# Kernel optimization log

Hardware: AMD Instinct MI355X
Metric: run time of the kernel (lower is better)

## Reference

```python
import jax, jax.numpy as jnp
import numpy as np

CH = 512
COND = 1280
HEADS = 8
GROUPS = CH // 8
EPS = 1e-5


def conv2d(x, w, b, pad):
    y = jax.lax.conv_general_dilated(
        x, w, window_strides=(1, 1), padding=[(pad, pad), (pad, pad)],
        dimension_numbers=('NCHW', 'OIHW', 'NCHW'))
    return y + b[None, :, None, None]


def group_norm(x, gamma, beta, groups, eps=EPS):
    b, c, h, w = x.shape
    xg = x.reshape(b, groups, c // groups, h, w)
    mu = xg.mean(axis=(2, 3, 4), keepdims=True)
    var = xg.var(axis=(2, 3, 4), keepdims=True)
    xn = ((xg - mu) * jax.lax.rsqrt(var + eps)).reshape(b, c, h, w)
    return xn * gamma[None, :, None, None] + beta[None, :, None, None]


def setup_inputs() -> dict:
    key = jax.random.key(0)
    ks = jax.random.split(key, 20)
    s = 0.05
    inp = {
        'x': jax.random.normal(ks[0], (8, CH, 32, 32), jnp.float32),
        'conditioning': jax.random.normal(ks[1], (8, COND), jnp.float32),
        # ResBlock params
        'c1w': jax.random.normal(ks[2], (CH, CH, 3, 3), jnp.float32) * s,
        'c1b': jnp.zeros((CH,), jnp.float32),
        'g1w': jnp.ones((CH,), jnp.float32),
        'g1b': jnp.zeros((CH,), jnp.float32),
        'c2w': jax.random.normal(ks[3], (CH, CH, 3, 3), jnp.float32) * s,
        'c2b': jnp.zeros((CH,), jnp.float32),
        'g2w': jnp.ones((CH,), jnp.float32),
        'g2b': jnp.zeros((CH,), jnp.float32),
        'cpw': jax.random.normal(ks[4], (CH, COND), jnp.float32) * s,
        'cpb': jnp.zeros((CH,), jnp.float32),
        'rpw': jax.random.normal(ks[5], (CH, CH, 1, 1), jnp.float32) * s,
        'rpb': jnp.zeros((CH,), jnp.float32),
        # Attention params (1x1 convs)
        'qw': jax.random.normal(ks[6], (CH, CH, 1, 1), jnp.float32) * s,
        'qb': jnp.zeros((CH,), jnp.float32),
        'kw': jax.random.normal(ks[7], (CH, CH, 1, 1), jnp.float32) * s,
        'kb': jnp.zeros((CH,), jnp.float32),
        'vw': jax.random.normal(ks[8], (CH, CH, 1, 1), jnp.float32) * s,
        'vb': jnp.zeros((CH,), jnp.float32),
        'ow': jax.random.normal(ks[9], (CH, CH, 1, 1), jnp.float32) * s,
        'ob': jnp.zeros((CH,), jnp.float32),
    }
    return inp


def reference(x, conditioning, c1w, c1b, g1w, g1b, c2w, c2b, g2w, g2b,
              cpw, cpb, rpw, rpb, qw, qb, kw, kb, vw, vb, ow, ob):
    # --- ResBlock ---
    residual = conv2d(x, rpw, rpb, 0)
    h = conv2d(x, c1w, c1b, 1)
    h = group_norm(h, g1w, g1b, GROUPS)
    h = jax.nn.silu(h)
    h = conv2d(h, c2w, c2b, 1)
    h = group_norm(h, g2w, g2b, GROUPS)
    cond = conditioning @ cpw.T + cpb  # [B, C]
    h = h * (1.0 + cond[:, :, None, None]) + residual

    # --- SpatialSelfAttention ---
    b, c, hh, ww = h.shape
    d = c // HEADS
    scale = d ** (-0.5)
    q = conv2d(h, qw, qb, 0).reshape(b, HEADS, d, hh * ww)
    k = conv2d(h, kw, kb, 0).reshape(b, HEADS, d, hh * ww)
    v = conv2d(h, vw, vb, 0).reshape(b, HEADS, d, hh * ww)
    attn = jnp.einsum('bhdn,bhdm->bhnm', q, k) * scale  # [B,H,N,N]
    attn = jax.nn.softmax(attn, axis=-1)
    out = jnp.einsum('bhnm,bhdm->bhdn', attn, v).reshape(b, c, hh, ww)
    return conv2d(out, ow, ob, 0) + h
```

## Files before the change

### kernel.cpp

```cpp
#include <hip/hip_runtime.h>
#include <hip/hip_bf16.h>

typedef unsigned short u16;
typedef unsigned long long u64;
typedef __attribute__((ext_vector_type(8))) short bf8;
typedef __attribute__((ext_vector_type(4))) short bf4;
typedef __attribute__((ext_vector_type(4))) float f32x4;

#define CH_ 512
#define NSP 1024
#define NB 8
#define CONDDIM 1280
#define NGROUP 64
#define HEADS_ 8
#define HD 64
#define PR 34
#define PPB (PR*PR)
#define QSCALE 0.18033688011112042f

#define VWAIT(N) asm volatile("s_waitcnt vmcnt(" #N ")" ::: "memory")
#define SCHEDB __builtin_amdgcn_sched_barrier(0)
#define BARRIER do { SCHEDB; __builtin_amdgcn_s_barrier(); SCHEDB; } while (0)

__device__ __forceinline__ u16 f2bf(float f) {
  union { float f; unsigned u; } v; v.f = f;
  unsigned u = v.u;
  return (u16)((u + 0x7fffu + ((u >> 16) & 1u)) >> 16);
}

__device__ __forceinline__ unsigned cvt_pk_bf16(float lo, float hi) {
  unsigned r;
  asm volatile("v_cvt_pk_bf16_f32 %0, %1, %2" : "=v"(r) : "v"(lo), "v"(hi));
  return r;
}

__device__ __forceinline__ f32x4 mfma_bf16(bf8 a, bf8 b, f32x4 c) {
  return __builtin_amdgcn_mfma_f32_16x16x32_bf16(a, b, c, 0, 0, 0);
}

__device__ __forceinline__ void gload16(const void* g, void* l) {
  __builtin_amdgcn_global_load_lds((const __attribute__((address_space(1))) void*)g,
                                   (__attribute__((address_space(3))) void*)l, 16, 0, 0);
}


__global__ __launch_bounds__(1024) void pack_x_kernel(const float* __restrict__ x, u16* __restrict__ xp) {
  __shared__ float t[32][33];
  int b = blockIdx.z;
  int c0 = blockIdx.y * 32, p0 = blockIdx.x * 32;
  int tx = threadIdx.x & 31, ty = threadIdx.x >> 5;
  t[ty][tx] = x[((size_t)b * CH_ + c0 + ty) * NSP + p0 + tx];
  __syncthreads();
  int p = p0 + ty;
  int y = p >> 5, xc = p & 31;
  xp[((size_t)b * PPB + (size_t)(y + 1) * PR + xc + 1) * CH_ + c0 + tx] = f2bf(t[tx][ty]);
}

__global__ __launch_bounds__(256) void border_zero_kernel(u16* __restrict__ a, u16* __restrict__ b) {
  int id = blockIdx.x * 256 + threadIdx.x;
  if (id >= NB * 132 * 64) return;
  int ch8 = id & 63;
  int rest = id >> 6;
  int bidx = rest % 132;
  int bb = rest / 132;
  int r, c;
  if (bidx < 34)       { r = 0;          c = bidx; }
  else if (bidx < 68)  { r = 33;         c = bidx - 34; }
  else if (bidx < 100) { r = bidx - 67;  c = 0; }
  else                 { r = bidx - 99;  c = 33; }
  size_t off = ((size_t)bb * PPB + (size_t)r * PR + c) * CH_ + ch8 * 8;
  const bf8 z = {0, 0, 0, 0, 0, 0, 0, 0};
  *(bf8*)(a + off) = z;
  *(bf8*)(b + off) = z;
}

__global__ __launch_bounds__(256) void pack_w3_kernel(const float* __restrict__ wA, const float* __restrict__ wB,
                                                      u16* __restrict__ dA, u16* __restrict__ dB) {
  int id = blockIdx.x * 256 + threadIdx.x;
  if (id >= 9 * 64 * CH_) return;
  const float* w = blockIdx.y ? wB : wA;
  u16* wp = blockIdx.y ? dB : dA;
  int co = id & (CH_ - 1);
  int cib = (id >> 9) & 63;
  int t = id >> 15;
  int dy = t / 3, dx = t % 3;
  bf8 v;
#pragma unroll
  for (int j = 0; j < 8; j++) {
    int ci = cib * 8 + j;
    v[j] = (short)f2bf(w[(((size_t)co * CH_ + ci) * 3 + dy) * 3 + dx]);
  }
  *(bf8*)(wp + ((size_t)(t * 64 + cib) * CH_ + co) * 8) = v;
}

__global__ __launch_bounds__(256) void pack_w1_kernel(
    const float* __restrict__ s0, const float* __restrict__ s1, const float* __restrict__ s2,
    const float* __restrict__ s3, const float* __restrict__ s4,
    u16* __restrict__ d0, u16* __restrict__ d1, u16* __restrict__ d2,
    u16* __restrict__ d3, u16* __restrict__ d4) {
  int id = blockIdx.x * 256 + threadIdx.x;
  if (id >= 64 * CH_) return;
  const float* w; u16* wp;
  switch (blockIdx.y) {
    case 0: w = s0; wp = d0; break;
    case 1: w = s1; wp = d1; break;
    case 2: w = s2; wp = d2; break;
    case 3: w = s3; wp = d3; break;
    default: w = s4; wp = d4; break;
  }
  int co = id & (CH_ - 1);
  int cib = id >> 9;
  bf8 v;
#pragma unroll
  for (int j = 0; j < 8; j++) v[j] = (short)f2bf(w[(size_t)co * CH_ + cib * 8 + j]);
  *(bf8*)(wp + ((size_t)cib * CH_ + co) * 8) = v;
}

__global__ __launch_bounds__(256) void cond_kernel(const float* __restrict__ cd, const float* __restrict__ cpw,
                                                   const float* __restrict__ cpb, float* __restrict__ cond) {
  int b = blockIdx.y;
  int c = blockIdx.x * 4 + (threadIdx.x >> 6);
  int lane = threadIdx.x & 63;
  const float* wrow = cpw + (size_t)c * CONDDIM;
  const float* crow = cd + (size_t)b * CONDDIM;
  float s = 0.f;
  for (int i = lane; i < CONDDIM; i += 64) s += crow[i] * wrow[i];
#pragma unroll
  for (int m = 32; m > 0; m >>= 1) s += __shfl_xor(s, m, 64);
  if (lane == 0) cond[b * CH_ + c] = s + cpb[c];
}

template <int TAPS, int PIN, int EPI>
__global__ __launch_bounds__(256, 3) void conv_kernel(
    const u16* __restrict__ in, const u16* __restrict__ wp, const float* __restrict__ bias,
    float* __restrict__ outf, const float* __restrict__ addf,
    u16* __restrict__ o0, u16* __restrict__ o1, u16* __restrict__ o2,
    const float* __restrict__ b0, const float* __restrict__ b1, const float* __restrict__ b2,
    const u16* __restrict__ wp2, float* __restrict__ outf2, const float* __restrict__ bias2) {
  constexpr int LDSZ = (TAPS == 9) ? (2 * 14336 + 3 * 12288 + (EPI == 6 ? 2 * 4096 : 0))
                                   : (4 * 8192 + 4 * 4096);
  __shared__ char lds[LDSZ];
  char* ldsA = lds;
  char* ldsB = lds + ((TAPS == 9) ? 2 * 14336 : 4 * 8192);
  char* ldsR = lds + 2 * 14336 + 3 * 12288;

  const int b = blockIdx.z;
  int seg = 0, coy = blockIdx.y;
  if constexpr (EPI == 5) { seg = coy >> 3; coy &= 7; }
  const int co0 = coy * 64;
  const int p0 = blockIdx.x * 128;
  const int tid = threadIdx.x;
  const int lane = tid & 63, wid = tid >> 6;
  const int wv = wid >> 1, wc = wid & 1;
  const int l15 = lane & 15, lhi = lane >> 4;

  const char* aSrc;
  if constexpr (TAPS == 9) {
    aSrc = (const char*)in + ((size_t)b * PPB + (size_t)blockIdx.x * 4 * PR) * 1024;
  } else if constexpr (PIN) {
    aSrc = (const char*)in + (size_t)b * PPB * 1024;
  } else {
    aSrc = (const char*)in + ((size_t)b * NSP + p0) * 1024;
  }
  const char* bSrc = (const char*)wp + (size_t)((EPI == 5) ? seg * 524288 : 0) + co0 * 16;
  const char* rSrc = (const char*)wp2 + co0 * 16;

  const int pB = ((tid >> 6) * 512 + (tid & 63)) * 16;
  int pA0, pA1, pA3 = 0;
  if constexpr (TAPS == 9) {
    int r0 = tid >> 2;
    int c0s = (tid & 3) ^ ((r0 >> 1) & 3);
    pA0 = (r0 << 10) + (c0s << 4);
    int r3 = 192 + ((tid & 127) >> 2);
    int c3s = (tid & 3) ^ ((r3 >> 1) & 3);
    pA3 = (r3 << 10) + (c3s << 4);
    pA1 = 0;
  } else {
    int a0 = (tid >> 2), a1 = 64 + (tid >> 2);
    int cs = (tid & 3) ^ (((tid >> 2) >> 1) & 3);
    if constexpr (PIN) {
      int pp0 = p0 + a0, pp1 = p0 + a1;
      int g0 = ((pp0 >> 5) + 1) * PR + (pp0 & 31) + 1;
      int g1 = ((pp1 >> 5) + 1) * PR + (pp1 & 31) + 1;
      pA0 = (g0 << 10) + (cs << 4);
      pA1 = (g1 << 10) + (cs << 4);
    } else {
      pA0 = (a0 << 10) + (cs << 4);
      pA1 = (a1 << 10) + (cs << 4);
    }
  }

  const int rowbA = (TAPS == 9) ? (wv * 68 + l15) : (wv * 64 + l15);
  const int aAddr = rowbA * 64 + ((lhi ^ ((l15 >> 1) & 3)) << 4);
  const int bAddr = (lhi * 64 + wc * 32 + l15) * 16;

  f32x4 acc[4][2], accR[4][2];
#pragma unroll
  for (int m = 0; m < 4; m++)
#pragma unroll
    for (int n = 0; n < 2; n++) { acc[m][n] = {0.f, 0.f, 0.f, 0.f}; accR[m][n] = {0.f, 0.f, 0.f, 0.f}; }

  if constexpr (TAPS == 9) {
    gload16(aSrc + pA0,          ldsA + (wid << 10));
    gload16(aSrc + pA0 + 65536,  ldsA + 4096 + (wid << 10));
    gload16(aSrc + pA0 + 131072, ldsA + 8192 + (wid << 10));
    gload16(aSrc + pA3,          ldsA + 12288 + ((wid & 1) << 10));
    gload16(bSrc + (size_t)(0 * 64) * 8192 + pB, ldsB + (wid << 10));
    gload16(bSrc + (size_t)(1 * 64) * 8192 + pB, ldsB + 4096 + (wid << 10));
    gload16(bSrc + (size_t)(2 * 64) * 8192 + pB, ldsB + 8192 + (wid << 10));
    gload16(bSrc + (size_t)(3 * 64) * 8192 + pB, ldsB + 12288 + (wid << 10));
    gload16(bSrc + (size_t)(4 * 64) * 8192 + pB, ldsB + 12288 + 4096 + (wid << 10));
    gload16(bSrc + (size_t)(5 * 64) * 8192 + pB, ldsB + 12288 + 8192 + (wid << 10));
    if constexpr (EPI == 6) {
      gload16(rSrc + pB, ldsR + (wid << 10));
      VWAIT(4);
    } else {
      VWAIT(3);
    }
    BARRIER;

#define AREAD(Ab_, K) (*(const bf8*)((Ab_) + (rowbA + (K)) * 64 + ((lhi ^ (((rowbA + (K)) >> 1) & 3)) << 4)))

#define PH3(KC, T, AS) do {                                                             \
    const int kcn_ = ((KC) < 15) ? (KC) + 1 : 15;                                       \
    if constexpr ((T) == 0) {                                                           \
      gload16(bSrc + (size_t)(6 * 64 + (KC) * 4) * 8192 + pB, ldsB + 24576 + (wid << 10)); \
      gload16(bSrc + (size_t)(7 * 64 + (KC) * 4) * 8192 + pB, ldsB + 24576 + 4096 + (wid << 10)); \
      gload16(bSrc + (size_t)(8 * 64 + (KC) * 4) * 8192 + pB, ldsB + 24576 + 8192 + (wid << 10)); \
      gload16(aSrc + kcn_ * 64 + pA0,         ldsA + (1 - (AS)) * 14336 + (wid << 10)); \
      gload16(aSrc + kcn_ * 64 + pA0 + 65536, ldsA + (1 - (AS)) * 14336 + 4096 + (wid << 10)); \
    } else if constexpr ((T) == 1) {                                                    \
      gload16(bSrc + (size_t)(0 * 64 + kcn_ * 4) * 8192 + pB, ldsB + (wid << 10));      \
      gload16(bSrc + (size_t)(1 * 64 + kcn_ * 4) * 8192 + pB, ldsB + 4096 + (wid << 10)); \
      gload16(bSrc + (size_t)(2 * 64 + kcn_ * 4) * 8192 + pB, ldsB + 8192 + (wid << 10)); \
      gload16(aSrc + kcn_ * 64 + pA0 + 131072, ldsA + (1 - (AS)) * 14336 + 8192 + (wid << 10)); \
      if constexpr (EPI == 6)                                                           \
        if ((KC) < 15)                                                                  \
          gload16(rSrc + (size_t)kcn_ * 32768 + pB, ldsR + (kcn_ & 1) * 4096 + (wid << 10)); \
    } else {                                                                            \
      gload16(bSrc + (size_t)(3 * 64 + kcn_ * 4) * 8192 + pB, ldsB + 12288 + (wid << 10)); \
      gload16(bSrc + (size_t)(4 * 64 + kcn_ * 4) * 8192 + pB, ldsB + 12288 + 4096 + (wid << 10)); \
      gload16(bSrc + (size_t)(5 * 64 + kcn_ * 4) * 8192 + pB, ldsB + 12288 + 8192 + (wid << 10)); \
      gload16(aSrc + kcn_ * 64 + pA3, ldsA + (1 - (AS)) * 14336 + 12288 + ((wid & 1) << 10)); \
    }                                                                                   \
    SCHEDB;                                                                             \
    {                                                                                   \
      const char* Ab_ = ldsA + (AS) * 14336;                                            \
      const char* Bb_ = ldsB + (T) * 12288;                                             \
      bf8 af_[3][4], bq_[3][2];                                                         \
      _Pragma("unroll")                                                                 \
      for (int tt = 0; tt < 3; tt++) {                                                  \
        const int DT_ = (T) * 34 + tt;                                                  \
        af_[tt][0] = AREAD(Ab_, DT_ + 0);                                               \
        af_[tt][1] = AREAD(Ab_, DT_ + 16);                                              \
        af_[tt][2] = AREAD(Ab_, DT_ + 34);                                              \
        af_[tt][3] = AREAD(Ab_, DT_ + 50);                                              \
        bq_[tt][0] = *(const bf8*)(Bb_ + tt * 4096 + 0   + bAddr);                      \
        bq_[tt][1] = *(const bf8*)(Bb_ + tt * 4096 + 256 + bAddr);                      \
      }                                                                                 \
      __builtin_amdgcn_s_setprio(1);                                                    \
      _Pragma("unroll")                                                                 \
      for (int tt = 0; tt < 3; tt++)                                                    \
        _Pragma("unroll")                                                               \
        for (int m = 0; m < 4; m++) {                                                   \
          acc[m][0] = mfma_bf16(af_[tt][m], bq_[tt][0], acc[m][0]);                     \
          acc[m][1] = mfma_bf16(af_[tt][m], bq_[tt][1], acc[m][1]);                     \
        }                                                                               \
      if constexpr (EPI == 6 && (T) == 1) {                                             \
        bf8 rq0 = *(const bf8*)(ldsR + ((KC) & 1) * 4096 + 0   + bAddr);                \
        bf8 rq1 = *(const bf8*)(ldsR + ((KC) & 1) * 4096 + 256 + bAddr);                \
        _Pragma("unroll")                                                               \
        for (int m = 0; m < 4; m++) {                                                   \
          accR[m][0] = mfma_bf16(af_[1][m], rq0, accR[m][0]);                           \
          accR[m][1] = mfma_bf16(af_[1][m], rq1, accR[m][1]);                           \
        }                                                                               \
      }                                                                                 \
      __builtin_amdgcn_s_setprio(0);                                                    \
    }                                                                                   \
    if constexpr ((T) == 0) { VWAIT(5); }                                               \
    else if constexpr ((T) == 1) {                                                      \
      if constexpr (EPI == 6) { VWAIT(5); } else { VWAIT(4); }                          \
    } else { VWAIT(4); }                                                                \
    BARRIER;                                                                            \
  } while (0)

    for (int kc2 = 0; kc2 < 8; kc2++) {
      PH3(kc2 * 2,     0, 0); PH3(kc2 * 2,     1, 0); PH3(kc2 * 2,     2, 0);
      PH3(kc2 * 2 + 1, 0, 1); PH3(kc2 * 2 + 1, 1, 1); PH3(kc2 * 2 + 1, 2, 1);
    }
#undef PH3
#undef AREAD
  } else {
    gload16(aSrc + pA0,         ldsA + (wid << 10));
    gload16(aSrc + pA1,         ldsA + 4096 + (wid << 10));
    gload16(bSrc + pB,          ldsB + (wid << 10));
    gload16(aSrc + 64 + pA0,    ldsA + 8192 + (wid << 10));
    gload16(aSrc + 64 + pA1,    ldsA + 8192 + 4096 + (wid << 10));
    gload16(bSrc + 32768 + pB,  ldsB + 4096 + (wid << 10));
    VWAIT(3);
    BARRIER;

#define PH1(KC, S) do {                                                                 \
    constexpr int S2 = ((S) + 2) & 3;                                                   \
    const int kcn_ = ((KC) + 2 < 16) ? (KC) + 2 : 15;                                   \
    gload16(bSrc + (size_t)kcn_ * 32768 + pB, ldsB + S2 * 4096 + (wid << 10));          \
    gload16(aSrc + kcn_ * 64 + pA0, ldsA + S2 * 8192 + (wid << 10));                    \
    gload16(aSrc + kcn_ * 64 + pA1, ldsA + S2 * 8192 + 4096 + (wid << 10));             \
    SCHEDB;                                                                             \
    bf8 af0 = *(const bf8*)(ldsA + (S) * 8192 + 0    + aAddr);                          \
    bf8 af1 = *(const bf8*)(ldsA + (S) * 8192 + 1024 + aAddr);                          \
    bf8 af2 = *(const bf8*)(ldsA + (S) * 8192 + 2048 + aAddr);                          \
    bf8 af3 = *(const bf8*)(ldsA + (S) * 8192 + 3072 + aAddr);                          \
    bf8 bq0 = *(const bf8*)(ldsB + (S) * 4096 + 0   + bAddr);                           \
    bf8 bq1 = *(const bf8*)(ldsB + (S) * 4096 + 256 + bAddr);                           \
    __builtin_amdgcn_s_setprio(1);                                                      \
    acc[0][0] = mfma_bf16(af0, bq0, acc[0][0]);                                         \
    acc[0][1] = mfma_bf16(af0, bq1, acc[0][1]);                                         \
    acc[1][0] = mfma_bf16(af1, bq0, acc[1][0]);                                         \
    acc[1][1] = mfma_bf16(af1, bq1, acc[1][1]);                                         \
    acc[2][0] = mfma_bf16(af2, bq0, acc[2][0]);                                         \
    acc[2][1] = mfma_bf16(af2, bq1, acc[2][1]);                                         \
    acc[3][0] = mfma_bf16(af3, bq0, acc[3][0]);                                         \
    acc[3][1] = mfma_bf16(af3, bq1, acc[3][1]);                                         \
    __builtin_amdgcn_s_setprio(0);                                                      \
    VWAIT(3);                                                                           \
    BARRIER;                                                                            \
  } while (0)

    for (int kc4 = 0; kc4 < 4; kc4++) {
      PH1(kc4 * 4 + 0, 0); PH1(kc4 * 4 + 1, 1); PH1(kc4 * 4 + 2, 2); PH1(kc4 * 4 + 3, 3);
    }
#undef PH1
  }

  VWAIT(0);

#pragma unroll
  for (int m = 0; m < 4; m++) {
    int pbase = p0 + wv * 64 + m * 16 + lhi * 4;
#pragma unroll
    for (int n = 0; n < 2; n++) {
      int co = co0 + wc * 32 + n * 16 + l15;
      if constexpr (EPI == 0) {
        float bv = bias[co];
#pragma unroll
        for (int r = 0; r < 4; r++)
          outf[((size_t)b * NSP + pbase + r) * CH_ + co] = acc[m][n][r] + bv;
      } else if constexpr (EPI == 6) {
        float bv = bias[co];
        float rv = bias2[co];
#pragma unroll
        for (int r = 0; r < 4; r++) {
          size_t idx = ((size_t)b * NSP + pbase + r) * CH_ + co;
          outf[idx]  = acc[m][n][r] + bv;
          outf2[idx] = accR[m][n][r] + rv;
        }
      } else if constexpr (EPI == 2) {
        float bv = bias[co];
        f32x4 v;
#pragma unroll
        for (int r = 0; r < 4; r++)
          v[r] = acc[m][n][r] + bv + addf[((size_t)b * NSP + pbase + r) * CH_ + co];
        *(f32x4*)(outf + ((size_t)b * CH_ + co) * NSP + pbase) = v;
      } else {
        if (seg == 0) {
          float bv = b0[co];
#pragma unroll
          for (int r = 0; r < 4; r++)
            o0[((size_t)b * NSP + pbase + r) * CH_ + co] = f2bf((acc[m][n][r] + bv) * QSCALE);
        } else if (seg == 1) {
          float bv = b1[co];
#pragma unroll
          for (int r = 0; r < 4; r++)
            o1[((size_t)b * NSP + pbase + r) * CH_ + co] = f2bf(acc[m][n][r] + bv);
        } else {
          float bv = b2[co];
          union { bf4 v; u64 u; } pk4;
#pragma unroll
          for (int r = 0; r < 4; r++) pk4.v[r] = (short)f2bf(acc[m][n][r] + bv);
          int np = (pbase & ~31) | ((pbase & 12) << 1) | ((pbase & 16) >> 2);
          *(u64*)(o2 + ((size_t)b * CH_ + co) * NSP + np) = pk4.u;
        }
      }
    }
  }
}

template <int MODE>
__global__ __launch_bounds__(256) void gn_kernel(
    const float* __restrict__ in, const float* __restrict__ gw, const float* __restrict__ gb,
    const float* __restrict__ cond, const float* __restrict__ resid,
    float* __restrict__ outf, u16* __restrict__ outb) {
  int b = blockIdx.y, g = blockIdx.x;
  int tid = threadIdx.x;
  int c = g * 8 + (tid & 7);
  int prow = tid >> 3;
  const float* base = in + (size_t)b * NSP * CH_ + c;
  float v[32];
  float s = 0.f, ss = 0.f;
#pragma unroll
  for (int i = 0; i < 32; i++) {
    v[i] = base[(size_t)(prow + i * 32) * CH_];
    s += v[i]; ss += v[i] * v[i];
  }
  __shared__ float rs[256], rss[256];
  rs[tid] = s; rss[tid] = ss;
  __syncthreads();
  for (int off = 128; off > 0; off >>= 1) {
    if (tid < off) { rs[tid] += rs[tid + off]; rss[tid] += rss[tid + off]; }
    __syncthreads();
  }
  float mean = rs[0] * (1.f / 8192.f);
  float var = rss[0] * (1.f / 8192.f) - mean * mean;
  float inv = rsqrtf(var + 1e-5f);
  float gamma = gw[c], beta = gb[c];
  float cm = 0.f;
  if (MODE == 1) cm = 1.f + cond[b * CH_ + c];
#pragma unroll
  for (int i = 0; i < 32; i++) {
    int p = prow + i * 32;
    float y = (v[i] - mean) * inv * gamma + beta;
    if (MODE == 0) {
      float sg = 1.f / (1.f + __expf(-y));
      int yy = p >> 5, xc = p & 31;
      outb[((size_t)b * PPB + (size_t)(yy + 1) * PR + xc + 1) * CH_ + c] = f2bf(y * sg);
    } else {
      size_t idx = ((size_t)b * NSP + p) * CH_ + c;
      float z = y * cm + resid[idx];
      outf[idx] = z;
      outb[idx] = f2bf(z);
    }
  }
}

__global__ __launch_bounds__(256, 2) void attn_kernel(const u16* __restrict__ q, const u16* __restrict__ k,
                                                      const u16* __restrict__ vT, u16* __restrict__ ao) {
  int bid = blockIdx.x;
  int swz = (bid & 7) * 64 + (bid >> 3);
  int b = swz >> 6;
  int head = (swz >> 3) & 7;
  int qt = swz & 7;
  int tid = threadIdx.x, lane = tid & 63, wid = tid >> 6;
  int l15 = lane & 15, lhi = lane >> 4;
  int cb = head * HD;
  int q0 = qt * 128 + wid * 32;

  const char* qp = (const char*)(q + (size_t)b * NSP * CH_ + cb);
  const char* kp = (const char*)(k + (size_t)b * NSP * CH_ + cb);
  const char* vp = (const char*)(vT + ((size_t)b * CH_ + cb) * NSP);

  __shared__ u16 Ksh[3][64 * 64];
  __shared__ u16 Vsh[3][64 * 64];

  bf8 aq[2][2];
#pragma unroll
  for (int qh = 0; qh < 2; qh++)
#pragma unroll
    for (int ks = 0; ks < 2; ks++)
      aq[qh][ks] = *(const bf8*)(qp + ((size_t)(q0 + qh * 16 + l15) * CH_ + ks * 32 + lhi * 8) * 2);

  const bf8 ones8 = {16256, 16256, 16256, 16256, 16256, 16256, 16256, 16256};

  f32x4 o[2][4], osum[2];
#pragma unroll
  for (int qh = 0; qh < 2; qh++) {
    osum[qh] = {0.f, 0.f, 0.f, 0.f};
#pragma unroll
    for (int n = 0; n < 4; n++) o[qh][n] = {0.f, 0.f, 0.f, 0.f};
  }

  auto stage = [&](int kt, int buf) {
#pragma unroll
    for (int t = 0; t < 2; t++) {
      int i = wid * 2 + t;
      int chunk = i * 64 + lane;
      int r = chunk >> 3, c = chunk & 7;
      gload16(kp + (size_t)(kt * 64 + r) * 1024 + (size_t)((c ^ (r & 7)) * 16),
              (char*)Ksh[buf] + i * 1024);
    }
#pragma unroll
    for (int t = 0; t < 2; t++) {
      int i = wid * 2 + t;
      int chunk = i * 64 + lane;
      int r = chunk >> 3, c = chunk & 7;
      gload16(vp + (size_t)r * 2048 + (size_t)(kt * 128) + (size_t)((c ^ (r & 7)) * 16),
              (char*)Vsh[buf] + i * 1024);
    }
  };

  auto qk = [&](int buf, f32x4 (&sacc)[2][4]) {
    const char* Kb = (const char*)Ksh[0] + buf * 8192;
#pragma unroll
    for (int qh = 0; qh < 2; qh++)
#pragma unroll
      for (int kf = 0; kf < 4; kf++) sacc[qh][kf] = {0.f, 0.f, 0.f, 0.f};
#pragma unroll
    for (int kf = 0; kf < 4; kf++) {
      bf8 ak[2];
#pragma unroll
      for (int ks = 0; ks < 2; ks++)
        ak[ks] = *(const bf8*)(Kb + (size_t)(kf * 16 + l15) * 128 + (((ks * 4 + lhi) ^ (l15 & 7)) * 16));
#pragma unroll
      for (int qh = 0; qh < 2; qh++)
#pragma unroll
        for (int ks = 0; ks < 2; ks++)
          sacc[qh][kf] = mfma_bf16(ak[ks], aq[qh][ks], sacc[qh][kf]);
    }
  };

  auto smpv = [&](int buf, f32x4 (&sacc)[2][4]) {
    const char* Vb = (const char*)Vsh[0] + buf * 8192;
    unsigned pk[2][4][2];
#pragma unroll
    for (int qh = 0; qh < 2; qh++)
#pragma unroll
      for (int kf = 0; kf < 4; kf++) {
        f32x4 pv;
#pragma unroll
        for (int r = 0; r < 4; r++) pv[r] = exp2f(sacc[qh][kf][r]);
        pk[qh][kf][0] = cvt_pk_bf16(pv[0], pv[1]);
        pk[qh][kf][1] = cvt_pk_bf16(pv[2], pv[3]);
      }
#pragma unroll
    for (int g = 0; g < 2; g++) {
      union { bf8 v8; unsigned u[4]; } ap[2];
#pragma unroll
      for (int qh = 0; qh < 2; qh++) {
        ap[qh].u[0] = pk[qh][2 * g][0];
        ap[qh].u[1] = pk[qh][2 * g][1];
        ap[qh].u[2] = pk[qh][2 * g + 1][0];
        ap[qh].u[3] = pk[qh][2 * g + 1][1];
      }
#pragma unroll
      for (int nf2 = 0; nf2 < 4; nf2++) {
        int row = nf2 * 16 + l15;
        bf8 bv8 = *(const bf8*)(Vb + (size_t)row * 128 + (((4 * g + lhi) ^ (l15 & 7)) * 16));
#pragma unroll
        for (int qh = 0; qh < 2; qh++)
          o[qh][nf2] = mfma_bf16(ap[qh].v8, bv8, o[qh][nf2]);
      }
#pragma unroll
      for (int qh = 0; qh < 2; qh++)
        osum[qh] = mfma_bf16(ap[qh].v8, ones8, osum[qh]);
    }
  };

  stage(0, 0);
  stage(1, 1);
  VWAIT(4);
  BARRIER;

  f32x4 saccA[2][4], saccB[2][4];
  qk(0, saccA);

  int bc = 0;
  for (int kt2 = 0; kt2 < 8; kt2++) {
    {
      int kt = 2 * kt2;
      int bn = (bc == 2) ? 0 : bc + 1;
      int bs = (bn == 2) ? 0 : bn + 1;
      VWAIT(0);
      BARRIER;
      qk(bn, saccB);
      if (kt < 14) stage(kt + 2, bs);
      smpv(bc, saccA);
      bc = bn;
    }
    {
      int kt = 2 * kt2 + 1;
      if (kt < 15) {
        int bn = (bc == 2) ? 0 : bc + 1;
        int bs = (bn == 2) ? 0 : bn + 1;
        VWAIT(0);
        BARRIER;
        qk(bn, saccA);
        if (kt < 14) stage(kt + 2, bs);
        smpv(bc, saccB);
        bc = bn;
      } else {
        smpv(bc, saccB);
      }
    }
  }

#pragma unroll
  for (int qh = 0; qh < 2; qh++) {
    float linv[4];
#pragma unroll
    for (int r = 0; r < 4; r++) linv[r] = 1.f / osum[qh][r];
#pragma unroll
    for (int nf2 = 0; nf2 < 4; nf2++)
#pragma unroll
      for (int r = 0; r < 4; r++) {
        float val = o[qh][nf2][r] * linv[r];
        ao[((size_t)b * NSP + q0 + qh * 16 + lhi * 4 + r) * CH_ + cb + nf2 * 16 + l15] = f2bf(val);
      }
  }
}


extern "C" void kernel_launch(void* const* d_in, const int* in_sizes, int n_in,
                              void* d_out, int out_size, void* d_ws, size_t ws_size,
                              hipStream_t stream) {
  const float* x    = (const float*)d_in[0];
  const float* cnd  = (const float*)d_in[1];
  const float* c1w  = (const float*)d_in[2];
  const float* c1b  = (const float*)d_in[3];
  const float* g1w  = (const float*)d_in[4];
  const float* g1b  = (const float*)d_in[5];
  const float* c2w  = (const float*)d_in[6];
  const float* c2b  = (const float*)d_in[7];
  const float* g2w  = (const float*)d_in[8];
  const float* g2b  = (const float*)d_in[9];
  const float* cpw  = (const float*)d_in[10];
  const float* cpb  = (const float*)d_in[11];
  const float* rpw  = (const float*)d_in[12];
  const float* rpb  = (const float*)d_in[13];
  const float* qw   = (const float*)d_in[14];
  const float* qb   = (const float*)d_in[15];
  const float* kw   = (const float*)d_in[16];
  const float* kb   = (const float*)d_in[17];
  const float* vw   = (const float*)d_in[18];
  const float* vb   = (const float*)d_in[19];
  const float* ow   = (const float*)d_in[20];
  const float* ob   = (const float*)d_in[21];
  float* out = (float*)d_out;

  char* ws = (char*)d_ws;
  size_t off = 0;
  auto alloc = [&](size_t bytes) -> char* {
    char* p = ws + off;
    off = (off + bytes + 255) & ~(size_t)255;
    return p;
  };
  const size_t ACT_F = (size_t)NB * NSP * CH_ * 4;
  const size_t ACT_B = (size_t)NB * NSP * CH_ * 2;
  const size_t PAD_B = (size_t)NB * PPB * CH_ * 2;

  u16* xp    = (u16*)alloc(PAD_B);
  u16* h1p   = (u16*)alloc(PAD_B);
  u16* w1p   = (u16*)alloc((size_t)9 * CH_ * CH_ * 2);
  u16* w2p   = (u16*)alloc((size_t)9 * CH_ * CH_ * 2);
  u16* wrp   = (u16*)alloc((size_t)CH_ * CH_ * 2);
  u16* wqkv  = (u16*)alloc((size_t)3 * CH_ * CH_ * 2);
  u16* wop   = (u16*)alloc((size_t)CH_ * CH_ * 2);
  float* cndv = (float*)alloc((size_t)NB * CH_ * 4);
  float* resid = (float*)alloc(ACT_F);
  float* h12  = (float*)alloc(ACT_F);
  u16* hb    = (u16*)alloc(ACT_B);
  u16* qbuf  = (u16*)alloc(ACT_B);
  u16* kbuf  = (u16*)alloc(ACT_B);
  u16* vTb   = (u16*)alloc(ACT_B);
  u16* aob   = (u16*)alloc(ACT_B);
  if (off > ws_size) return;

  dim3 tgrid(NSP / 32, CH_ / 32, NB);
  border_zero_kernel<<<(NB * 132 * 64 + 255) / 256, 256, 0, stream>>>(xp, h1p);
  pack_x_kernel<<<tgrid, 1024, 0, stream>>>(x, xp);
  pack_w3_kernel<<<dim3((9 * 64 * CH_ + 255) / 256, 2), 256, 0, stream>>>(c1w, c2w, w1p, w2p);
  pack_w1_kernel<<<dim3((64 * CH_) / 256, 5), 256, 0, stream>>>(
      rpw, qw, kw, vw, ow,
      wrp, wqkv, wqkv + (size_t)CH_ * CH_, wqkv + (size_t)2 * CH_ * CH_, wop);
  cond_kernel<<<dim3(CH_ / 4, NB), 256, 0, stream>>>(cnd, cpw, cpb, cndv);

  dim3 ggrid(NSP / 128, CH_ / 64, NB);
  dim3 qgrid(NSP / 128, 3 * CH_ / 64, NB);
  conv_kernel<9, 1, 6><<<ggrid, 256, 0, stream>>>(xp, w1p, c1b, h12, nullptr,
                                                  nullptr, nullptr, nullptr, nullptr, nullptr, nullptr,
                                                  wrp, resid, rpb);
  gn_kernel<0><<<dim3(NGROUP, NB), 256, 0, stream>>>(h12, g1w, g1b, nullptr, nullptr, nullptr, h1p);
  conv_kernel<9, 1, 0><<<ggrid, 256, 0, stream>>>(h1p, w2p, c2b, h12, nullptr,
                                                  nullptr, nullptr, nullptr, nullptr, nullptr, nullptr,
                                                  nullptr, nullptr, nullptr);
  gn_kernel<1><<<dim3(NGROUP, NB), 256, 0, stream>>>(h12, g2w, g2b, cndv, resid, h12, hb);
  conv_kernel<1, 0, 5><<<qgrid, 256, 0, stream>>>(hb, wqkv, nullptr, nullptr, nullptr,
                                                  qbuf, kbuf, vTb, qb, kb, vb,
                                                  nullptr, nullptr, nullptr);
  attn_kernel<<<512, 256, 0, stream>>>(qbuf, kbuf, vTb, aob);
  conv_kernel<1, 0, 2><<<ggrid, 256, 0, stream>>>(aob, wop, ob, out, h12,
                                                  nullptr, nullptr, nullptr, nullptr, nullptr, nullptr,
                                                  nullptr, nullptr, nullptr);
}
```

Baseline: 239.1 us.

## Merge prep kernels into one launch and store conv outputs as bf16 for groupnorm

Five setup kernels (border zeroing, input packing, weight packing and the conditioning projection) become a single prep_kernel launch that dispatches on block index. The two 3x3 convs now write bf16 pre-norm activations instead of fp32, which halves the traffic into the groupnorm kernels. The groupnorm kernels are rewritten to load 8 channels per thread as 16-byte vectors and store vectorized outputs. The cost is bf16 rounding before the groupnorm statistics, which may reduce accuracy.

Result: faster. 221.3 us (-7.4%).

```diff
diff --git a/kernel.cpp b/kernel.cpp
--- a/kernel.cpp
+++ b/kernel.cpp
@@ -28,6 +28,10 @@
   return (u16)((u + 0x7fffu + ((u >> 16) & 1u)) >> 16);
 }
 
+__device__ __forceinline__ float b2f(u16 x) {
+  union { unsigned u; float f; } v; v.u = ((unsigned)x) << 16; return v.f;
+}
+
 __device__ __forceinline__ unsigned cvt_pk_bf16(float lo, float hi) {
   unsigned r;
   asm volatile("v_cvt_pk_bf16_f32 %0, %1, %2" : "=v"(r) : "v"(lo), "v"(hi));
@@ -43,91 +47,99 @@
                                    (__attribute__((address_space(3))) void*)l, 16, 0, 0);
 }
 
-
-__global__ __launch_bounds__(1024) void pack_x_kernel(const float* __restrict__ x, u16* __restrict__ xp) {
+__global__ __launch_bounds__(256) void prep_kernel(
+    const float* __restrict__ x, u16* __restrict__ xp, u16* __restrict__ h1p,
+    const float* __restrict__ c1w, const float* __restrict__ c2w,
+    u16* __restrict__ w1p, u16* __restrict__ w2p,
+    const float* __restrict__ rpw, const float* __restrict__ qw, const float* __restrict__ kw,
+    const float* __restrict__ vw, const float* __restrict__ ow,
+    u16* __restrict__ wrp, u16* __restrict__ wq, u16* __restrict__ wk,
+    u16* __restrict__ wv, u16* __restrict__ wo,
+    const float* __restrict__ cd, const float* __restrict__ cpw,
+    const float* __restrict__ cpb, float* __restrict__ cond) {
   __shared__ float t[32][33];
-  int b = blockIdx.z;
-  int c0 = blockIdx.y * 32, p0 = blockIdx.x * 32;
-  int tx = threadIdx.x & 31, ty = threadIdx.x >> 5;
-  t[ty][tx] = x[((size_t)b * CH_ + c0 + ty) * NSP + p0 + tx];
-  __syncthreads();
-  int p = p0 + ty;
-  int y = p >> 5, xc = p & 31;
-  xp[((size_t)b * PPB + (size_t)(y + 1) * PR + xc + 1) * CH_ + c0 + tx] = f2bf(t[tx][ty]);
-}
-
-__global__ __launch_bounds__(256) void border_zero_kernel(u16* __restrict__ a, u16* __restrict__ b) {
-  int id = blockIdx.x * 256 + threadIdx.x;
-  if (id >= NB * 132 * 64) return;
-  int ch8 = id & 63;
-  int rest = id >> 6;
-  int bidx = rest % 132;
-  int bb = rest / 132;
-  int r, c;
-  if (bidx < 34)       { r = 0;          c = bidx; }
-  else if (bidx < 68)  { r = 33;         c = bidx - 34; }
-  else if (bidx < 100) { r = bidx - 67;  c = 0; }
-  else                 { r = bidx - 99;  c = 33; }
-  size_t off = ((size_t)bb * PPB + (size_t)r * PR + c) * CH_ + ch8 * 8;
-  const bf8 z = {0, 0, 0, 0, 0, 0, 0, 0};
-  *(bf8*)(a + off) = z;
-  *(bf8*)(b + off) = z;
-}
-
-__global__ __launch_bounds__(256) void pack_w3_kernel(const float* __restrict__ wA, const float* __restrict__ wB,
-                                                      u16* __restrict__ dA, u16* __restrict__ dB) {
-  int id = blockIdx.x * 256 + threadIdx.x;
-  if (id >= 9 * 64 * CH_) return;
-  const float* w = blockIdx.y ? wB : wA;
-  u16* wp = blockIdx.y ? dB : dA;
-  int co = id & (CH_ - 1);
-  int cib = (id >> 9) & 63;
-  int t = id >> 15;
-  int dy = t / 3, dx = t % 3;
-  bf8 v;
-#pragma unroll
-  for (int j = 0; j < 8; j++) {
-    int ci = cib * 8 + j;
-    v[j] = (short)f2bf(w[(((size_t)co * CH_ + ci) * 3 + dy) * 3 + dx]);
-  }
-  *(bf8*)(wp + ((size_t)(t * 64 + cib) * CH_ + co) * 8) = v;
-}
-
-__global__ __launch_bounds__(256) void pack_w1_kernel(
-    const float* __restrict__ s0, const float* __restrict__ s1, const float* __restrict__ s2,
-    const float* __restrict__ s3, const float* __restrict__ s4,
-    u16* __restrict__ d0, u16* __restrict__ d1, u16* __restrict__ d2,
-    u16* __restrict__ d3, u16* __restrict__ d4) {
-  int id = blockIdx.x * 256 + threadIdx.x;
-  if (id >= 64 * CH_) return;
-  const float* w; u16* wp;
-  switch (blockIdx.y) {
-    case 0: w = s0; wp = d0; break;
-    case 1: w = s1; wp = d1; break;
-    case 2: w = s2; wp = d2; break;
-    case 3: w = s3; wp = d3; break;
-    default: w = s4; wp = d4; break;
-  }
-  int co = id & (CH_ - 1);
-  int cib = id >> 9;
-  bf8 v;
-#pragma unroll
-  for (int j = 0; j < 8; j++) v[j] = (short)f2bf(w[(size_t)co * CH_ + cib * 8 + j]);
-  *(bf8*)(wp + ((size_t)cib * CH_ + co) * 8) = v;
-}
-
-__global__ __launch_bounds__(256) void cond_kernel(const float* __restrict__ cd, const float* __restrict__ cpw,
-                                                   const float* __restrict__ cpb, float* __restrict__ cond) {
-  int b = blockIdx.y;
-  int c = blockIdx.x * 4 + (threadIdx.x >> 6);
-  int lane = threadIdx.x & 63;
-  const float* wrow = cpw + (size_t)c * CONDDIM;
-  const float* crow = cd + (size_t)b * CONDDIM;
-  float s = 0.f;
-  for (int i = lane; i < CONDDIM; i += 64) s += crow[i] * wrow[i];
-#pragma unroll
-  for (int m = 32; m > 0; m >>= 1) s += __shfl_xor(s, m, 64);
-  if (lane == 0) cond[b * CH_ + c] = s + cpb[c];
+  int bid = blockIdx.x;
+  int tid = threadIdx.x;
+  if (bid < 4096) {
+    int px = bid & 31, py = (bid >> 5) & 15, b = bid >> 9;
+    int c0 = py * 32, p0 = px * 32;
+    int tx = tid & 31, ty = tid >> 5;
+#pragma unroll
+    for (int i = 0; i < 4; i++) {
+      int row = ty + i * 8;
+      t[row][tx] = x[((size_t)b * CH_ + c0 + row) * NSP + p0 + tx];
+    }
+    __syncthreads();
+#pragma unroll
+    for (int i = 0; i < 4; i++) {
+      int pr = ty + i * 8;
+      int p = p0 + pr;
+      int y = p >> 5, xc = p & 31;
+      xp[((size_t)b * PPB + (size_t)(y + 1) * PR + xc + 1) * CH_ + c0 + tx] = f2bf(t[tx][pr]);
+    }
+  } else if (bid < 4360) {
+    int id = (bid - 4096) * 256 + tid;
+    int ch8 = id & 63;
+    int rest = id >> 6;
+    int bidx = rest % 132;
+    int bb = rest / 132;
+    int r, c;
+    if (bidx < 34)       { r = 0;          c = bidx; }
+    else if (bidx < 68)  { r = 33;         c = bidx - 34; }
+    else if (bidx < 100) { r = bidx - 67;  c = 0; }
+    else                 { r = bidx - 99;  c = 33; }
+    size_t off = ((size_t)bb * PPB + (size_t)r * PR + c) * CH_ + ch8 * 8;
+    const bf8 z = {0, 0, 0, 0, 0, 0, 0, 0};
+    *(bf8*)(xp + off) = z;
+    *(bf8*)(h1p + off) = z;
+  } else if (bid < 6664) {
+    int id2 = bid - 4360;
+    int which = (id2 >= 1152) ? 1 : 0;
+    int id = (id2 - which * 1152) * 256 + tid;
+    const float* w = which ? c2w : c1w;
+    u16* wp = which ? w2p : w1p;
+    int co = id & (CH_ - 1);
+    int cib = (id >> 9) & 63;
+    int tt = id >> 15;
+    int dy = tt / 3, dx = tt % 3;
+    bf8 v;
+#pragma unroll
+    for (int j = 0; j < 8; j++) {
+      int ci = cib * 8 + j;
+      v[j] = (short)f2bf(w[(((size_t)co * CH_ + ci) * 3 + dy) * 3 + dx]);
+    }
+    *(bf8*)(wp + ((size_t)(tt * 64 + cib) * CH_ + co) * 8) = v;
+  } else if (bid < 7304) {
+    int id3 = bid - 6664;
+    int which = id3 >> 7;
+    int id = (id3 & 127) * 256 + tid;
+    const float* w; u16* wp;
+    switch (which) {
+      case 0: w = rpw; wp = wrp; break;
+      case 1: w = qw;  wp = wq;  break;
+      case 2: w = kw;  wp = wk;  break;
+      case 3: w = vw;  wp = wv;  break;
+      default: w = ow; wp = wo;  break;
+    }
+    int co = id & (CH_ - 1);
+    int cib = id >> 9;
+    bf8 v;
+#pragma unroll
+    for (int j = 0; j < 8; j++) v[j] = (short)f2bf(w[(size_t)co * CH_ + cib * 8 + j]);
+    *(bf8*)(wp + ((size_t)cib * CH_ + co) * 8) = v;
+  } else {
+    int id4 = bid - 7304;
+    int b = id4 >> 7;
+    int c = (id4 & 127) * 4 + (tid >> 6);
+    int lane = tid & 63;
+    const float* wrow = cpw + (size_t)c * CONDDIM;
+    const float* crow = cd + (size_t)b * CONDDIM;
+    float s = 0.f;
+    for (int i = lane; i < CONDDIM; i += 64) s += crow[i] * wrow[i];
+#pragma unroll
+    for (int m = 32; m > 0; m >>= 1) s += __shfl_xor(s, m, 64);
+    if (lane == 0) cond[b * CH_ + c] = s + cpb[c];
+  }
 }
 
 template <int TAPS, int PIN, int EPI>
@@ -137,7 +149,7 @@
     u16* __restrict__ o0, u16* __restrict__ o1, u16* __restrict__ o2,
     const float* __restrict__ b0, const float* __restrict__ b1, const float* __restrict__ b2,
     const u16* __restrict__ wp2, float* __restrict__ outf2, const float* __restrict__ bias2) {
-  constexpr int LDSZ = (TAPS == 9) ? (2 * 14336 + 3 * 12288 + (EPI == 6 ? 2 * 4096 : 0))
+  constexpr int LDSZ = (TAPS == 9) ? (2 * 14336 + 3 * 12288 + (EPI == 8 ? 2 * 4096 : 0))
                                    : (4 * 8192 + 4 * 4096);
   __shared__ char lds[LDSZ];
   char* ldsA = lds;
@@ -211,7 +223,7 @@
     gload16(bSrc + (size_t)(3 * 64) * 8192 + pB, ldsB + 12288 + (wid << 10));
     gload16(bSrc + (size_t)(4 * 64) * 8192 + pB, ldsB + 12288 + 4096 + (wid << 10));
     gload16(bSrc + (size_t)(5 * 64) * 8192 + pB, ldsB + 12288 + 8192 + (wid << 10));
-    if constexpr (EPI == 6) {
+    if constexpr (EPI == 8) {
       gload16(rSrc + pB, ldsR + (wid << 10));
       VWAIT(4);
     } else {
@@ -234,7 +246,7 @@
       gload16(bSrc + (size_t)(1 * 64 + kcn_ * 4) * 8192 + pB, ldsB + 4096 + (wid << 10)); \
       gload16(bSrc + (size_t)(2 * 64 + kcn_ * 4) * 8192 + pB, ldsB + 8192 + (wid << 10)); \
       gload16(aSrc + kcn_ * 64 + pA0 + 131072, ldsA + (1 - (AS)) * 14336 + 8192 + (wid << 10)); \
-      if constexpr (EPI == 6)                                                           \
+      if constexpr (EPI == 8)                                                           \
         if ((KC) < 15)                                                                  \
           gload16(rSrc + (size_t)kcn_ * 32768 + pB, ldsR + (kcn_ & 1) * 4096 + (wid << 10)); \
     } else {                                                                            \
@@ -266,7 +278,7 @@
           acc[m][0] = mfma_bf16(af_[tt][m], bq_[tt][0], acc[m][0]);                     \
           acc[m][1] = mfma_bf16(af_[tt][m], bq_[tt][1], acc[m][1]);                     \
         }                                                                               \
-      if constexpr (EPI == 6 && (T) == 1) {                                             \
+      if constexpr (EPI == 8 && (T) == 1) {                                             \
         bf8 rq0 = *(const bf8*)(ldsR + ((KC) & 1) * 4096 + 0   + bAddr);                \
         bf8 rq1 = *(const bf8*)(ldsR + ((KC) & 1) * 4096 + 256 + bAddr);                \
         _Pragma("unroll")                                                               \
@@ -279,7 +291,7 @@
     }                                                                                   \
     if constexpr ((T) == 0) { VWAIT(5); }                                               \
     else if constexpr ((T) == 1) {                                                      \
-      if constexpr (EPI == 6) { VWAIT(5); } else { VWAIT(4); }                          \
+      if constexpr (EPI == 8) { VWAIT(5); } else { VWAIT(4); }                          \
     } else { VWAIT(4); }                                                                \
     BARRIER;                                                                            \
   } while (0)
@@ -341,18 +353,18 @@
 #pragma unroll
     for (int n = 0; n < 2; n++) {
       int co = co0 + wc * 32 + n * 16 + l15;
-      if constexpr (EPI == 0) {
+      if constexpr (EPI == 7) {
         float bv = bias[co];
 #pragma unroll
         for (int r = 0; r < 4; r++)
-          outf[((size_t)b * NSP + pbase + r) * CH_ + co] = acc[m][n][r] + bv;
-      } else if constexpr (EPI == 6) {
+          o0[((size_t)b * NSP + pbase + r) * CH_ + co] = f2bf(acc[m][n][r] + bv);
+      } else if constexpr (EPI == 8) {
         float bv = bias[co];
         float rv = bias2[co];
 #pragma unroll
         for (int r = 0; r < 4; r++) {
           size_t idx = ((size_t)b * NSP + pbase + r) * CH_ + co;
-          outf[idx]  = acc[m][n][r] + bv;
+          o0[idx]    = f2bf(acc[m][n][r] + bv);
           outf2[idx] = accR[m][n][r] + rv;
         }
       } else if constexpr (EPI == 2) {
@@ -388,20 +400,20 @@
 
 template <int MODE>
 __global__ __launch_bounds__(256) void gn_kernel(
-    const float* __restrict__ in, const float* __restrict__ gw, const float* __restrict__ gb,
+    const u16* __restrict__ in, const float* __restrict__ gw, const float* __restrict__ gb,
     const float* __restrict__ cond, const float* __restrict__ resid,
     float* __restrict__ outf, u16* __restrict__ outb) {
   int b = blockIdx.y, g = blockIdx.x;
   int tid = threadIdx.x;
-  int c = g * 8 + (tid & 7);
-  int prow = tid >> 3;
-  const float* base = in + (size_t)b * NSP * CH_ + c;
-  float v[32];
+  const u16* base = in + (size_t)b * NSP * CH_ + g * 8;
+  bf8 v[4];
   float s = 0.f, ss = 0.f;
 #pragma unroll
-  for (int i = 0; i < 32; i++) {
-    v[i] = base[(size_t)(prow + i * 32) * CH_];
-    s += v[i]; ss += v[i] * v[i];
+  for (int i = 0; i < 4; i++) {
+    int p = tid + i * 256;
+    v[i] = *(const bf8*)(base + (size_t)p * CH_);
+#pragma unroll
+    for (int j = 0; j < 8; j++) { float f = b2f((u16)v[i][j]); s += f; ss += f * f; }
   }
   __shared__ float rs[256], rss[256];
   rs[tid] = s; rss[tid] = ss;
@@ -413,22 +425,50 @@
   float mean = rs[0] * (1.f / 8192.f);
   float var = rss[0] * (1.f / 8192.f) - mean * mean;
   float inv = rsqrtf(var + 1e-5f);
-  float gamma = gw[c], beta = gb[c];
-  float cm = 0.f;
-  if (MODE == 1) cm = 1.f + cond[b * CH_ + c];
-#pragma unroll
-  for (int i = 0; i < 32; i++) {
-    int p = prow + i * 32;
-    float y = (v[i] - mean) * inv * gamma + beta;
+  float gam[8], bet[8], cm[8];
+  *(f32x4*)(gam)     = *(const f32x4*)(gw + g * 8);
+  *(f32x4*)(gam + 4) = *(const f32x4*)(gw + g * 8 + 4);
+  *(f32x4*)(bet)     = *(const f32x4*)(gb + g * 8);
+  *(f32x4*)(bet + 4) = *(const f32x4*)(gb + g * 8 + 4);
+  if (MODE == 1) {
+    *(f32x4*)(cm)     = *(const f32x4*)(cond + b * CH_ + g * 8);
+    *(f32x4*)(cm + 4) = *(const f32x4*)(cond + b * CH_ + g * 8 + 4);
+#pragma unroll
+    for (int j = 0; j < 8; j++) cm[j] += 1.f;
+  }
+#pragma unroll
+  for (int i = 0; i < 4; i++) {
+    int p = tid + i * 256;
     if (MODE == 0) {
-      float sg = 1.f / (1.f + __expf(-y));
+      bf8 ov;
+#pragma unroll
+      for (int j = 0; j < 8; j++) {
+        float y = (b2f((u16)v[i][j]) - mean) * inv * gam[j] + bet[j];
+        float sg = 1.f / (1.f + __expf(-y));
+        ov[j] = (short)f2bf(y * sg);
+      }
       int yy = p >> 5, xc = p & 31;
-      outb[((size_t)b * PPB + (size_t)(yy + 1) * PR + xc + 1) * CH_ + c] = f2bf(y * sg);
+      *(bf8*)(outb + ((size_t)b * PPB + (size_t)(yy + 1) * PR + xc + 1) * CH_ + g * 8) = ov;
     } else {
-      size_t idx = ((size_t)b * NSP + p) * CH_ + c;
-      float z = y * cm + resid[idx];
-      outf[idx] = z;
-      outb[idx] = f2bf(z);
+      size_t idx = ((size_t)b * NSP + p) * CH_ + g * 8;
+      f32x4 r0 = *(const f32x4*)(resid + idx);
+      f32x4 r1 = *(const f32x4*)(resid + idx + 4);
+      f32x4 z0, z1; bf8 ov;
+#pragma unroll
+      for (int j = 0; j < 4; j++) {
+        float y = (b2f((u16)v[i][j]) - mean) * inv * gam[j] + bet[j];
+        z0[j] = y * cm[j] + r0[j];
+        ov[j] = (short)f2bf(z0[j]);
+      }
+#pragma unroll
+      for (int j = 0; j < 4; j++) {
+        float y = (b2f((u16)v[i][4 + j]) - mean) * inv * gam[4 + j] + bet[4 + j];
+        z1[j] = y * cm[4 + j] + r1[j];
+        ov[4 + j] = (short)f2bf(z1[j]);
+      }
+      *(f32x4*)(outf + idx)     = z0;
+      *(f32x4*)(outf + idx + 4) = z1;
+      *(bf8*)(outb + idx) = ov;
     }
   }
 }
@@ -654,25 +694,24 @@
   u16* aob   = (u16*)alloc(ACT_B);
   if (off > ws_size) return;
 
-  dim3 tgrid(NSP / 32, CH_ / 32, NB);
-  border_zero_kernel<<<(NB * 132 * 64 + 255) / 256, 256, 0, stream>>>(xp, h1p);
-  pack_x_kernel<<<tgrid, 1024, 0, stream>>>(x, xp);
-  pack_w3_kernel<<<dim3((9 * 64 * CH_ + 255) / 256, 2), 256, 0, stream>>>(c1w, c2w, w1p, w2p);
-  pack_w1_kernel<<<dim3((64 * CH_) / 256, 5), 256, 0, stream>>>(
-      rpw, qw, kw, vw, ow,
-      wrp, wqkv, wqkv + (size_t)CH_ * CH_, wqkv + (size_t)2 * CH_ * CH_, wop);
-  cond_kernel<<<dim3(CH_ / 4, NB), 256, 0, stream>>>(cnd, cpw, cpb, cndv);
+  u16* actb = aob;
+
+  prep_kernel<<<8328, 256, 0, stream>>>(x, xp, h1p, c1w, c2w, w1p, w2p,
+                                        rpw, qw, kw, vw, ow,
+                                        wrp, wqkv, wqkv + (size_t)CH_ * CH_,
+                                        wqkv + (size_t)2 * CH_ * CH_, wop,
+                                        cnd, cpw, cpb, cndv);
 
   dim3 ggrid(NSP / 128, CH_ / 64, NB);
   dim3 qgrid(NSP / 128, 3 * CH_ / 64, NB);
-  conv_kernel<9, 1, 6><<<ggrid, 256, 0, stream>>>(xp, w1p, c1b, h12, nullptr,
-                                                  nullptr, nullptr, nullptr, nullptr, nullptr, nullptr,
+  conv_kernel<9, 1, 8><<<ggrid, 256, 0, stream>>>(xp, w1p, c1b, nullptr, nullptr,
+                                                  actb, nullptr, nullptr, nullptr, nullptr, nullptr,
                                                   wrp, resid, rpb);
-  gn_kernel<0><<<dim3(NGROUP, NB), 256, 0, stream>>>(h12, g1w, g1b, nullptr, nullptr, nullptr, h1p);
-  conv_kernel<9, 1, 0><<<ggrid, 256, 0, stream>>>(h1p, w2p, c2b, h12, nullptr,
-                                                  nullptr, nullptr, nullptr, nullptr, nullptr, nullptr,
+  gn_kernel<0><<<dim3(NGROUP, NB), 256, 0, stream>>>(actb, g1w, g1b, nullptr, nullptr, nullptr, h1p);
+  conv_kernel<9, 1, 7><<<ggrid, 256, 0, stream>>>(h1p, w2p, c2b, nullptr, nullptr,
+                                                  actb, nullptr, nullptr, nullptr, nullptr, nullptr,
                                                   nullptr, nullptr, nullptr);
-  gn_kernel<1><<<dim3(NGROUP, NB), 256, 0, stream>>>(h12, g2w, g2b, cndv, resid, h12, hb);
+  gn_kernel<1><<<dim3(NGROUP, NB), 256, 0, stream>>>(actb, g2w, g2b, cndv, resid, h12, hb);
   conv_kernel<1, 0, 5><<<qgrid, 256, 0, stream>>>(hb, wqkv, nullptr, nullptr, nullptr,
                                                   qbuf, kbuf, vTb, qb, kb, vb,
                                                   nullptr, nullptr, nullptr);
```
